# Optimization experiments

Measured on AMD Instinct MI355X. Metric: run time of the kernel, lower is better.

The kernel has to match this reference:

```python
import jax, jax.numpy as jnp
import numpy as np

K = 20
EPS = 1e-5

def get_graph_feature(x, k):
    # x: [B, C, N] -> edge features [B, 2C, N, k]
    xt = jnp.swapaxes(x, 1, 2)  # [B, N, C]
    sq = jnp.sum(xt * xt, axis=-1)  # [B, N]
    # negative squared distance: -(|a|^2 + |b|^2 - 2 a.b)
    pair = 2.0 * jnp.einsum('bnc,bmc->bnm', xt, xt) - sq[:, :, None] - sq[:, None, :]
    idx = jax.lax.top_k(pair, k)[1]  # [B, N, k] nearest neighbors (incl. self)
    neigh = jax.vmap(lambda f, i: f[i])(xt, idx)  # [B, N, k, C]
    ctr = xt[:, :, None, :]  # [B, N, 1, C]
    edge = jnp.concatenate([neigh - ctr, jnp.broadcast_to(ctr, neigh.shape)], axis=-1)  # [B,N,k,2C]
    return jnp.transpose(edge, (0, 3, 1, 2))  # [B, 2C, N, k]

def bn_lrelu(y, g, b, axes):
    # training-mode batchnorm (biased batch stats) + LeakyReLU(0.2)
    m = jnp.mean(y, axis=axes, keepdims=True)
    v = jnp.var(y, axis=axes, keepdims=True)
    shape = [1, -1] + [1] * (y.ndim - 2)
    yn = (y - m) / jnp.sqrt(v + EPS) * g.reshape(shape) + b.reshape(shape)
    return jnp.where(yn >= 0, yn, 0.2 * yn)

def edge_block(x, w, g, b, k):
    e = get_graph_feature(x, k)           # [B, 2C, N, k]
    y = jnp.einsum('bcnk,oc->bonk', e, w)  # 1x1 conv2d, no bias
    y = bn_lrelu(y, g, b, (0, 2, 3))
    return jnp.max(y, axis=-1)            # max over k -> [B, O, N]

def setup_inputs() -> dict:
    key = jax.random.key(0)
    ks = jax.random.split(key, 8)
    B, N = 8, 1024
    num_features = 256
    def w(k_, o, i):
        return jax.random.normal(k_, (o, i), dtype=jnp.float32) * (1.0 / np.sqrt(i))
    d = {
        'x': jax.random.normal(ks[0], (B, N, 3), dtype=jnp.float32),
        'w1': w(ks[1], 64, 6),   'g1': jnp.ones(64),  'b1': jnp.zeros(64),
        'w2': w(ks[2], 64, 128), 'g2': jnp.ones(64),  'b2': jnp.zeros(64),
        'w3': w(ks[3], 128, 128),'g3': jnp.ones(128), 'b3': jnp.zeros(128),
        'w4': w(ks[4], 256, 256),'g4': jnp.ones(256), 'b4': jnp.zeros(256),
        'w5': w(ks[5], 512, 512),'g5': jnp.ones(512), 'b5': jnp.zeros(512),
        'wemb': w(ks[6], num_features, 512),
    }
    return d

def reference(x, w1, g1, b1, w2, g2, b2, w3, g3, b3, w4, g4, b4, w5, g5, b5, wemb):
    xc = jnp.swapaxes(x, 2, 1)  # [B, 3, N]
    x1 = edge_block(xc, w1, g1, b1, K)  # [B, 64, N]
    x2 = edge_block(x1, w2, g2, b2, K)  # [B, 64, N]
    x3 = edge_block(x2, w3, g3, b3, K)  # [B, 128, N]
    x4 = edge_block(x3, w4, g4, b4, K)  # [B, 256, N]
    cat = jnp.concatenate([x1, x2, x3, x4], axis=1)  # [B, 512, N]
    y = jnp.einsum('bcn,oc->bon', cat, w5)            # 1x1 conv1d
    y = bn_lrelu(y, g5, b5, (0, 2))
    feat = jnp.max(y, axis=-1)  # [B, 512]
    return feat @ wemb.T        # [B, num_features]
```

## Files before the change

### kernel.cpp

```cpp
#include <hip/hip_runtime.h>
#include <hip/hip_bf16.h>
#include <math.h>

#define BB 8
#define NN 1024
#define KNNK 20
#define LDC 512

typedef __attribute__((ext_vector_type(8))) short bfrag8;
typedef __attribute__((ext_vector_type(4))) float facc4;
typedef __attribute__((ext_vector_type(2))) float v2f;

struct bh8 { __hip_bfloat16 h[8]; };

__device__ __forceinline__ bh8 cvt8(float4 a, float4 b) {
    bh8 v;
    v.h[0] = __float2bfloat16(a.x); v.h[1] = __float2bfloat16(a.y);
    v.h[2] = __float2bfloat16(a.z); v.h[3] = __float2bfloat16(a.w);
    v.h[4] = __float2bfloat16(b.x); v.h[5] = __float2bfloat16(b.y);
    v.h[6] = __float2bfloat16(b.z); v.h[7] = __float2bfloat16(b.w);
    return v;
}

template<int CTRL, int RMASK>
__device__ __forceinline__ float fmax_dpp(float x) {
    int xi = __float_as_int(x);
    int yi = __builtin_amdgcn_update_dpp(xi, xi, CTRL, RMASK, 0xF, false);
    return fmaxf(x, __int_as_float(yi));
}

__device__ __forceinline__ float wave_max64(float x) {
    x = fmax_dpp<0x121, 0xF>(x);
    x = fmax_dpp<0x122, 0xF>(x);
    x = fmax_dpp<0x124, 0xF>(x);
    x = fmax_dpp<0x128, 0xF>(x);
    x = fmax_dpp<0x142, 0xA>(x);
    x = fmax_dpp<0x143, 0xC>(x);
    return __int_as_float(__builtin_amdgcn_readlane(__float_as_int(x), 63));
}

__device__ __forceinline__ void select20_pf(float (*dist)[1024],
                                            int q0, int w, int lane,
                                            int* __restrict__ idxout) {
    float d[2][16];
    int   sl[2][16];
#pragma unroll
    for (int qi = 0; qi < 2; qi++) {
        int row = w * 2 + qi;
#pragma unroll
        for (int j = 0; j < 16; j++) { d[qi][j] = dist[row][lane + 64 * j]; sl[qi][j] = j; }
    }
    constexpr unsigned char CA[63] = {
        0,2,4,6,8,10,12,14,
        0,1,4,5,8,9,12,13,
        1,5,9,13,
        0,1,2,3,8,9,10,11,
        2,3,10,11,
        1,3,5,9,11,13,
        0,1,2,3,4,5,6,7,
        4,5,6,7,
        2,3,6,7,10,11,
        1,3,5,7,9,11,13};
    constexpr unsigned char CB[63] = {
        1,3,5,7,9,11,13,15,
        2,3,6,7,10,11,14,15,
        2,6,10,14,
        4,5,6,7,12,13,14,15,
        4,5,12,13,
        2,4,6,10,12,14,
        8,9,10,11,12,13,14,15,
        8,9,10,11,
        4,5,8,9,12,13,
        2,4,6,8,10,12,14};
#pragma unroll
    for (int c = 0; c < 63; c++) {
        const int a = CA[c], bq = CB[c];
#pragma unroll
        for (int qi = 0; qi < 2; qi++) {
            bool sw = d[qi][a] < d[qi][bq];
            float dmx = sw ? d[qi][bq] : d[qi][a];
            float dmn = sw ? d[qi][a]  : d[qi][bq];
            d[qi][a] = dmx; d[qi][bq] = dmn;
            int smx = sw ? sl[qi][bq] : sl[qi][a];
            int smn = sw ? sl[qi][a]  : sl[qi][bq];
            sl[qi][a] = smx; sl[qi][bq] = smn;
        }
    }
    unsigned long long slp[2];
#pragma unroll
    for (int qi = 0; qi < 2; qi++) {
        int row = w * 2 + qi;
#pragma unroll
        for (int j = 0; j < 16; j++) dist[row][j * 64 + lane] = d[qi][j];
        unsigned long long p = 0;
#pragma unroll
        for (int j = 0; j < 16; j++) p |= (unsigned long long)sl[qi][j] << (4 * j);
        slp[qi] = p;
    }
    float head[2] = {d[0][0], d[1][0]};
    float pf[2]   = {d[0][1], d[1][1]};
    int   ptr[2]  = {2, 2};
    for (int t = 0; t < KNNK; t++) {
#pragma unroll
        for (int qi = 0; qi < 2; qi++) {
            int row = w * 2 + qi;
            float bv = wave_max64(head[qi]);
            unsigned long long ball = __ballot(head[qi] == bv);
            int wl = (int)__builtin_ctzll(ball);
            bool win = (lane == wl);
            if (win) {
                idxout[(q0 + row) * KNNK + t] = (int)(slp[qi] & 15ull) * 64 + lane;
            }
            head[qi] = win ? pf[qi] : head[qi];
            slp[qi]  = win ? (slp[qi] >> 4) : slp[qi];
            if (win) {
                int p = ptr[qi];
                pf[qi] = (p < 16) ? dist[row][p * 64 + lane] : -INFINITY;
                ptr[qi] = p + 1;
            }
        }
    }
}

__device__ __forceinline__ void zero_r1(float* r1s, float* r1q, int O, int tid) {
    for (int i = tid; i < 32 * O; i += 256) { r1s[i] = 0.f; r1q[i] = 0.f; }
}

__global__ __launch_bounds__(256, 4) void knn3_fused(const float* __restrict__ x,
                                                     const float* __restrict__ w1,
                                                     float* __restrict__ zf,
                                                     int* __restrict__ idxout,
                                                     float* __restrict__ r1s, float* __restrict__ r1q) {
    __shared__ float dist[8][1024];
    int tid = threadIdx.x;
    int q0 = (blockIdx.x & 7) * 1024 + (blockIdx.x >> 3) * 8;
    int b = q0 >> 10;
    if (blockIdx.x == 0) zero_r1(r1s, r1q, 64, tid);
    const float* xb = x + (size_t)b * NN * 3;
    int lane = tid & 63, w = tid >> 6;
    float qx[8], qy[8], qz[8];
#pragma unroll
    for (int q = 0; q < 8; q++) {
        const float* qr = xb + (size_t)((q0 & (NN - 1)) + q) * 3;
        qx[q] = qr[0]; qy[q] = qr[1]; qz[q] = qr[2];
    }
#pragma unroll
    for (int cq = 0; cq < 4; cq++) {
        int cand = w * 256 + cq * 64 + lane;
        const float* cr = xb + (size_t)cand * 3;
        float cx = cr[0], cy = cr[1], cz = cr[2];
        float sqc = 0.f;
        sqc += cx * cx; sqc += cy * cy; sqc += cz * cz;
#pragma unroll
        for (int q = 0; q < 8; q++) {
            float d = qx[q] * cx + qy[q] * cy + qz[q] * cz;
            dist[q][cand] = 2.f * d - sqc;
        }
    }
    for (int i = tid; i < 8 * 128; i += 256) {
        int lq = i >> 7, j = i & 127;
        const float* wr = w1 + (j < 64 ? j * 6 : (j - 64) * 6 + 3);
        const float* xr = x + (size_t)(q0 + lq) * 3;
        zf[(size_t)(q0 + lq) * 128 + j] = wr[0] * xr[0] + wr[1] * xr[1] + wr[2] * xr[2];
    }
    __syncthreads();
    select20_pf(dist, q0, w, lane, idxout);
}

template<int C>
__device__ __forceinline__ void knn_body(const float* __restrict__ xT,
                                         const float* __restrict__ sqn,
                                         int* __restrict__ idxout,
                                         float (*dist)[1024], int knnBlk) {
    int tid = threadIdx.x;
    int q0 = (knnBlk & 7) * 1024 + (knnBlk >> 3) * 8;
    int b = q0 >> 10;
    int lane = tid & 63, w = tid >> 6;
    int cand0 = w * 256 + 4 * lane;
    const float* xTb = xT + (size_t)b * C * 1024;
    const float* qrow = xTb + (q0 & (NN - 1));
    float4 sq4 = *(const float4*)(sqn + b * NN + cand0);
    v2f acc2[4][4];
#pragma unroll
    for (int j = 0; j < 4; j++)
#pragma unroll
        for (int p = 0; p < 4; p++) acc2[j][p] = (v2f){0.f, 0.f};
    for (int cg = 0; cg < C / 4; cg++) {
        float4 rch[4];
#pragma unroll
        for (int c = 0; c < 4; c++)
            rch[c] = *(const float4*)(xTb + (size_t)(4 * cg + c) * 1024 + cand0);
#pragma unroll
        for (int c = 0; c < 4; c++) {
            const float* qr = qrow + (size_t)(4 * cg + c) * 1024;
            float4 qa = *(const float4*)qr;
            float4 qb = *(const float4*)(qr + 4);
            v2f qp[4] = {{qa.x, qa.y}, {qa.z, qa.w}, {qb.x, qb.y}, {qb.z, qb.w}};
            float rj[4] = {rch[c].x, rch[c].y, rch[c].z, rch[c].w};
#pragma unroll
            for (int j = 0; j < 4; j++) {
                v2f rr = {rj[j], rj[j]};
                acc2[j][0] += rr * qp[0];
                acc2[j][1] += rr * qp[1];
                acc2[j][2] += rr * qp[2];
                acc2[j][3] += rr * qp[3];
            }
        }
    }
#pragma unroll
    for (int p = 0; p < 4; p++)
#pragma unroll
        for (int half = 0; half < 2; half++) {
            int q = 2 * p + half;
            float4 dv;
            dv.x = 2.f * acc2[0][p][half] - sq4.x;
            dv.y = 2.f * acc2[1][p][half] - sq4.y;
            dv.z = 2.f * acc2[2][p][half] - sq4.z;
            dv.w = 2.f * acc2[3][p][half] - sq4.w;
            *(float4*)&dist[q][cand0] = dv;
        }
    __syncthreads();
    select20_pf(dist, q0, w, lane, idxout);
}

template<int C, int ZO2>
__global__ __launch_bounds__(256, 4) void knnz_fat(const float* __restrict__ xT,
                                                   const float* __restrict__ xt, int off,
                                                   const float* __restrict__ sqn,
                                                   int* __restrict__ idxout,
                                                   const float* __restrict__ w,
                                                   float* __restrict__ zf,
                                                   float* __restrict__ r1s, float* __restrict__ r1q,
                                                   int Onext) {
    __shared__ float dist[8][1024];
    int tid = threadIdx.x;
    if ((int)blockIdx.x < BB * NN / 8) {
        knn_body<C>(xT, sqn, idxout, dist, blockIdx.x);
        return;
    }
    constexpr int ZO = ZO2 / 2;
    int zblk = blockIdx.x - BB * NN / 8;
    if (zblk == 0) zero_r1(r1s, r1q, Onext, tid);
    float (*xs)[C] = (float (*)[C])&dist[0][0];
    int p0 = zblk * 16;
    for (int j = tid; j < 16 * (C / 4); j += 256) {
        int p = j / (C / 4), c4 = j % (C / 4);
        *(float4*)&xs[p][4 * c4] = *(const float4*)(xt + (size_t)(p0 + p) * LDC + off + 4 * c4);
    }
    __syncthreads();
    for (int j = tid; j < ZO2; j += 256) {
        const float* wr = w + (j < ZO ? (size_t)j * 2 * C : (size_t)(j - ZO) * 2 * C + C);
        float acc[16];
#pragma unroll
        for (int p = 0; p < 16; p++) acc[p] = 0.f;
        for (int c4 = 0; c4 < C / 4; c4++) {
            float4 wv = *(const float4*)(wr + 4 * c4);
#pragma unroll
            for (int p = 0; p < 16; p++) {
                float4 xv = *(const float4*)&xs[p][4 * c4];
                acc[p] += wv.x * xv.x + wv.y * xv.y + wv.z * xv.z + wv.w * xv.w;
            }
        }
#pragma unroll
        for (int p = 0; p < 16; p++) zf[(size_t)(p0 + p) * ZO2 + j] = acc[p];
    }
}

__global__ __launch_bounds__(256, 4) void knnz4_fat(const float* __restrict__ xT,
                                                    const float* __restrict__ sqn,
                                                    int* __restrict__ idxout,
                                                    const float* __restrict__ xtcat,
                                                    const float* __restrict__ w4,
                                                    __hip_bfloat16* __restrict__ zf4,
                                                    float* __restrict__ r1s, float* __restrict__ r1q) {
    __shared__ __align__(16) char smem[36864];
    int tid = threadIdx.x;
    if ((int)blockIdx.x < BB * NN / 8) {
        float (*dist)[1024] = (float (*)[1024])smem;
        if (blockIdx.x == 0) zero_r1(r1s, r1q, 256, tid);
        knn_body<128>(xT, sqn, idxout, dist, blockIdx.x);
        return;
    }
    __hip_bfloat16 (*A)[72] = (__hip_bfloat16 (*)[72])smem;
    __hip_bfloat16 (*W)[72] = (__hip_bfloat16 (*)[72])(smem + 18432);
    int zblk = blockIdx.x - BB * NN / 8;
    int mt = zblk >> 2, nt = zblk & 3;
    int lane = tid & 63, wvx = tid >> 6;
    int mw = wvx >> 1, nw = wvx & 1;
    int m0 = lane & 15, qd = lane >> 4;
    int r = tid & 127, hf = tid >> 7;
    facc4 acc[4][4];
    facc4 zz = {0.f, 0.f, 0.f, 0.f};
#pragma unroll
    for (int mi = 0; mi < 4; mi++)
#pragma unroll
        for (int ni = 0; ni < 4; ni++) acc[mi][ni] = zz;
    int j = nt * 128 + r;
    const float* wsrc = w4 + (j < 256 ? (size_t)j * 256 : (size_t)(j - 256) * 256 + 128);
    const float* asrc = xtcat + (size_t)(mt * 128 + r) * 512 + 128;
    for (int kc = 0; kc < 2; kc++) {
#pragma unroll
        for (int u = 0; u < 4; u++) {
            int c0 = kc * 64 + hf * 32 + 8 * u;
            float4 a0 = *(const float4*)(asrc + c0);
            float4 a1 = *(const float4*)(asrc + c0 + 4);
            *(bh8*)&A[r][hf * 32 + 8 * u] = cvt8(a0, a1);
            float4 w0 = *(const float4*)(wsrc + c0);
            float4 w1 = *(const float4*)(wsrc + c0 + 4);
            *(bh8*)&W[r][hf * 32 + 8 * u] = cvt8(w0, w1);
        }
        __syncthreads();
#pragma unroll
        for (int kk = 0; kk < 2; kk++) {
            bfrag8 af[4], bf[4];
#pragma unroll
            for (int mi = 0; mi < 4; mi++)
                af[mi] = *(const bfrag8*)&A[64 * mw + 16 * mi + m0][32 * kk + 8 * qd];
#pragma unroll
            for (int ni = 0; ni < 4; ni++)
                bf[ni] = *(const bfrag8*)&W[64 * nw + 16 * ni + m0][32 * kk + 8 * qd];
#pragma unroll
            for (int mi = 0; mi < 4; mi++)
#pragma unroll
                for (int ni = 0; ni < 4; ni++)
                    acc[mi][ni] = __builtin_amdgcn_mfma_f32_16x16x32_bf16(af[mi], bf[ni], acc[mi][ni], 0, 0, 0);
        }
        __syncthreads();
    }
#pragma unroll
    for (int mi = 0; mi < 4; mi++)
#pragma unroll
        for (int ni = 0; ni < 4; ni++)
#pragma unroll
            for (int rg = 0; rg < 4; rg++) {
                int row = mt * 128 + mw * 64 + mi * 16 + qd * 4 + rg;
                int col = nt * 128 + nw * 64 + ni * 16 + m0;
                zf4[(size_t)row * 512 + col] = __float2bfloat16(acc[mi][ni][rg]);
            }
}

template<int O2>
__global__ __launch_bounds__(256) void gatherstats_k(const float* __restrict__ zf,
                                                     const int* __restrict__ idx,
                                                     float* __restrict__ ymax, float* __restrict__ ymin,
                                                     float* __restrict__ r1s, float* __restrict__ r1q) {
    constexpr int O = O2 / 2;
    __shared__ float red_s[4][O], red_q[4][O];
    int wv = threadIdx.x >> 6, lane = threadIdx.x & 63;
    int n = (blockIdx.x & 7) * 1024 + (blockIdx.x >> 3) * 4 + wv;
    int b = n >> 10;
    const float* zbatch = zf + (size_t)b * NN * O2;
    int nb[KNNK];
#pragma unroll
    for (int k = 0; k < KNNK; k++) nb[k] = idx[n * KNNK + k];
#pragma unroll
    for (int ch = 0; ch < O / 64; ch++) {
        int o = ch * 64 + lane;
        float g[KNNK];
#pragma unroll
        for (int k = 0; k < KNNK; k++) g[k] = zbatch[(size_t)nb[k] * O2 + o];
        float mx = -INFINITY, mn = INFINITY, s = 0.f, ss = 0.f;
#pragma unroll
        for (int k = 0; k < KNNK; k++) {
            float v = g[k];
            mx = fmaxf(mx, v); mn = fminf(mn, v); s += v; ss += v * v;
        }
        float zn  = zf[(size_t)n * O2 + o];
        float zbn = zf[(size_t)n * O2 + O + o];
        float d = zbn - zn;
        mx += d; mn += d;
        ss = ss + 2.f * d * s + (float)KNNK * d * d;
        s  = s + (float)KNNK * d;
        ymax[(size_t)n * O + o] = mx;
        ymin[(size_t)n * O + o] = mn;
        red_s[wv][o] = s;
        red_q[wv][o] = ss;
    }
    __syncthreads();
    int bucket = blockIdx.x & 31;
    for (int o = threadIdx.x; o < O; o += 256) {
        float s4 = red_s[0][o] + red_s[1][o] + red_s[2][o] + red_s[3][o];
        float q4 = red_q[0][o] + red_q[1][o] + red_q[2][o] + red_q[3][o];
        atomicAdd(&r1s[(size_t)bucket * O + o], s4);
        atomicAdd(&r1q[(size_t)bucket * O + o], q4);
    }
}

__global__ __launch_bounds__(256) void gatherstats4_k(const __hip_bfloat16* __restrict__ zf4,
                                                      const int* __restrict__ idx,
                                                      float* __restrict__ ymax, float* __restrict__ ymin,
                                                      float* __restrict__ r1s, float* __restrict__ r1q) {
    __shared__ float red_s[4][256], red_q[4][256];
    int wv = threadIdx.x >> 6, lane = threadIdx.x & 63;
    int n = (blockIdx.x & 7) * 1024 + (blockIdx.x >> 3) * 4 + wv;
    int b = n >> 10;
    const __hip_bfloat16* zbatch = zf4 + (size_t)b * NN * 512;
    int nb[KNNK];
#pragma unroll
    for (int k = 0; k < KNNK; k++) nb[k] = idx[n * KNNK + k];
#pragma unroll
    for (int ch = 0; ch < 4; ch++) {
        int o = ch * 64 + lane;
        float g[KNNK];
#pragma unroll
        for (int k = 0; k < KNNK; k++) g[k] = __bfloat162float(zbatch[(size_t)nb[k] * 512 + o]);
        float mx = -INFINITY, mn = INFINITY, s = 0.f, ss = 0.f;
#pragma unroll
        for (int k = 0; k < KNNK; k++) {
            float v = g[k];
            mx = fmaxf(mx, v); mn = fminf(mn, v); s += v; ss += v * v;
        }
        float zn  = __bfloat162float(zf4[(size_t)n * 512 + o]);
        float zbn = __bfloat162float(zf4[(size_t)n * 512 + 256 + o]);
        float d = zbn - zn;
        mx += d; mn += d;
        ss = ss + 2.f * d * s + (float)KNNK * d * d;
        s  = s + (float)KNNK * d;
        ymax[(size_t)n * 256 + o] = mx;
        ymin[(size_t)n * 256 + o] = mn;
        red_s[wv][o] = s;
        red_q[wv][o] = ss;
    }
    __syncthreads();
    int bucket = blockIdx.x & 31;
    for (int o = threadIdx.x; o < 256; o += 256) {
        float s4 = red_s[0][o] + red_s[1][o] + red_s[2][o] + red_s[3][o];
        float q4 = red_q[0][o] + red_q[1][o] + red_q[2][o] + red_q[3][o];
        atomicAdd(&r1s[(size_t)bucket * 256 + o], s4);
        atomicAdd(&r1q[(size_t)bucket * 256 + o], q4);
    }
}

template<int O>
__global__ __launch_bounds__(256) void epitrans2_k(const float* __restrict__ ymax, const float* __restrict__ ymin,
                                                   const float* __restrict__ r1s, const float* __restrict__ r1q,
                                                   const float* __restrict__ g, const float* __restrict__ beta,
                                                   double invM,
                                                   float* __restrict__ xtcat, int off_out,
                                                   float* __restrict__ xT, float* __restrict__ sqn,
                                                   __hip_bfloat16* __restrict__ xbf) {
    __shared__ float tile[64][O + 1];
    __shared__ float ssh[O], tth[O];
    int n0 = blockIdx.x * 64;
    int b = n0 >> 10;
    int tid = threadIdx.x;
    for (int o = tid; o < O; o += 256) {
        double sd = 0.0, qd = 0.0;
        for (int r = 0; r < 32; r++) { sd += r1s[(size_t)r * O + o]; qd += r1q[(size_t)r * O + o]; }
        double mean = sd * invM;
        double var = qd * invM - mean * mean;
        float inv = (float)(1.0 / sqrt(var + 1e-5));
        float sc = g[o] * inv;
        ssh[o] = sc;
        tth[o] = beta[o] - (float)mean * sc;
    }
    __syncthreads();
    for (int i = tid; i < 64 * O; i += 256) {
        int nl = i / O;
        int o = i & (O - 1);
        int n = n0 + nl;
        float sc = ssh[o];
        float v = sc >= 0.f ? ymax[(size_t)n * O + o] : ymin[(size_t)n * O + o];
        float y = sc * v + tth[o];
        y = y >= 0.f ? y : 0.2f * y;
        xtcat[(size_t)n * LDC + off_out + o] = y;
        xbf[(size_t)n * LDC + off_out + o] = __float2bfloat16(y);
        tile[nl][o] = y;
    }
    __syncthreads();
    if (tid < 64) {
        float sq = 0.f;
        for (int c = 0; c < O; c++) { float v = tile[tid][c]; sq += v * v; }
        sqn[n0 + tid] = sq;
    }
    int r = tid >> 4, cq = tid & 15;
#pragma unroll
    for (int ct = 0; ct < O / 16; ct++) {
        int c = ct * 16 + r;
        float4 ov;
        ov.x = tile[4 * cq + 0][c];
        ov.y = tile[4 * cq + 1][c];
        ov.z = tile[4 * cq + 2][c];
        ov.w = tile[4 * cq + 3][c];
        *(float4*)(xT + ((size_t)b * O + c) * 1024 + (n0 & (NN - 1)) + 4 * cq) = ov;
    }
}

__global__ __launch_bounds__(256) void epilogue4_k(const float* __restrict__ ymax, const float* __restrict__ ymin,
                                                   const float* __restrict__ r1s, const float* __restrict__ r1q,
                                                   const float* __restrict__ g, const float* __restrict__ beta,
                                                   double invM,
                                                   __hip_bfloat16* __restrict__ xbf) {
    __shared__ float ssh[256], tth[256];
    int n0 = blockIdx.x * 64;
    int tid = threadIdx.x;
    {
        int o = tid;
        double sd = 0.0, qd = 0.0;
        for (int r = 0; r < 32; r++) { sd += r1s[(size_t)r * 256 + o]; qd += r1q[(size_t)r * 256 + o]; }
        double mean = sd * invM;
        double var = qd * invM - mean * mean;
        float inv = (float)(1.0 / sqrt(var + 1e-5));
        float sc = g[o] * inv;
        ssh[o] = sc;
        tth[o] = beta[o] - (float)mean * sc;
    }
    __syncthreads();
    for (int i = tid; i < 64 * 256; i += 256) {
        int nl = i >> 8;
        int o = i & 255;
        int n = n0 + nl;
        float sc = ssh[o];
        float v = sc >= 0.f ? ymax[(size_t)n * 256 + o] : ymin[(size_t)n * 256 + o];
        float y = sc * v + tth[o];
        y = y >= 0.f ? y : 0.2f * y;
        xbf[(size_t)n * LDC + 256 + o] = __float2bfloat16(y);
    }
}

__global__ __launch_bounds__(256) void gemm5_mfma(const __hip_bfloat16* __restrict__ xbf,
                                                  const float* __restrict__ w5,
                                                  float* __restrict__ pmax, float* __restrict__ pmn,
                                                  float* __restrict__ ps, float* __restrict__ pq) {
    __shared__ __hip_bfloat16 A[128][72];
    __shared__ __hip_bfloat16 W[128][72];
    int mt = blockIdx.x >> 2, nt = blockIdx.x & 3;
    int tid = threadIdx.x;
    int lane = tid & 63, wvx = tid >> 6;
    int mw = wvx >> 1, nw = wvx & 1;
    int m0 = lane & 15, qd = lane >> 4;
    int r = tid & 127, hf = tid >> 7;
    facc4 acc[4][4];
    facc4 zz = {0.f, 0.f, 0.f, 0.f};
#pragma unroll
    for (int mi = 0; mi < 4; mi++)
#pragma unroll
        for (int ni = 0; ni < 4; ni++) acc[mi][ni] = zz;
    for (int kc = 0; kc < 8; kc++) {
        const __hip_bfloat16* ap = xbf + (size_t)(mt * 128 + r) * 512 + kc * 64 + hf * 32;
        const float* wp = w5 + (size_t)(nt * 128 + r) * 512 + kc * 64 + hf * 32;
#pragma unroll
        for (int u = 0; u < 4; u++) {
            bh8 av = *(const bh8*)(ap + 8 * u);
            *(bh8*)&A[r][hf * 32 + 8 * u] = av;
            float4 w0 = *(const float4*)(wp + 8 * u);
            float4 w1 = *(const float4*)(wp + 8 * u + 4);
            *(bh8*)&W[r][hf * 32 + 8 * u] = cvt8(w0, w1);
        }
        __syncthreads();
#pragma unroll
        for (int kk = 0; kk < 2; kk++) {
            bfrag8 af[4], bf[4];
#pragma unroll
            for (int mi = 0; mi < 4; mi++)
                af[mi] = *(const bfrag8*)&A[64 * mw + 16 * mi + m0][32 * kk + 8 * qd];
#pragma unroll
            for (int ni = 0; ni < 4; ni++)
                bf[ni] = *(const bfrag8*)&W[64 * nw + 16 * ni + m0][32 * kk + 8 * qd];
#pragma unroll
            for (int mi = 0; mi < 4; mi++)
#pragma unroll
                for (int ni = 0; ni < 4; ni++)
                    acc[mi][ni] = __builtin_amdgcn_mfma_f32_16x16x32_bf16(af[mi], bf[ni], acc[mi][ni], 0, 0, 0);
        }
        __syncthreads();
    }
#pragma unroll
    for (int mi = 0; mi < 4; mi++) {
        int grp = mt * 8 + mw * 4 + mi;
#pragma unroll
        for (int ni = 0; ni < 4; ni++) {
            float mx = -INFINITY, mn = INFINITY, s = 0.f, ss = 0.f;
#pragma unroll
            for (int rg = 0; rg < 4; rg++) {
                float v = acc[mi][ni][rg];
                mx = fmaxf(mx, v); mn = fminf(mn, v); s += v; ss += v * v;
            }
#pragma unroll
            for (int m = 16; m < 64; m <<= 1) {
                mx = fmaxf(mx, __shfl_xor(mx, m));
                mn = fminf(mn, __shfl_xor(mn, m));
                s += __shfl_xor(s, m);
                ss += __shfl_xor(ss, m);
            }
            if (qd == 0) {
                int o = nt * 128 + nw * 64 + ni * 16 + m0;
                pmax[(size_t)grp * 512 + o] = mx;
                pmn [(size_t)grp * 512 + o] = mn;
                ps  [(size_t)grp * 512 + o] = s;
                pq  [(size_t)grp * 512 + o] = ss;
            }
        }
    }
}

__global__ __launch_bounds__(256) void bnstat5_k(const float* __restrict__ ps, const float* __restrict__ pq,
                                                 const float* __restrict__ g, const float* __restrict__ beta,
                                                 float* __restrict__ s_out, float* __restrict__ t_out) {
    __shared__ double lds_s[4][8], lds_q[4][8];
    int tid = threadIdx.x;
    int lane = tid & 63, wv = tid >> 6;
    int ol = lane & 7;
    int rg = wv * 8 + (lane >> 3);
    int o = blockIdx.x * 8 + ol;
    double s = 0.0, q = 0.0;
    for (int r = rg; r < 512; r += 32) {
        s += ps[(size_t)r * 512 + o];
        q += pq[(size_t)r * 512 + o];
    }
    s += __shfl_xor(s, 8);  q += __shfl_xor(q, 8);
    s += __shfl_xor(s, 16); q += __shfl_xor(q, 16);
    s += __shfl_xor(s, 32); q += __shfl_xor(q, 32);
    if (lane < 8) { lds_s[wv][ol] = s; lds_q[wv][ol] = q; }
    __syncthreads();
    if (tid < 8) {
        s = lds_s[0][tid] + lds_s[1][tid] + lds_s[2][tid] + lds_s[3][tid];
        q = lds_q[0][tid] + lds_q[1][tid] + lds_q[2][tid] + lds_q[3][tid];
        double invM = 1.0 / (BB * NN);
        double mean = s * invM;
        double var = q * invM - mean * mean;
        float inv = (float)(1.0 / sqrt(var + 1e-5));
        int oo = blockIdx.x * 8 + tid;
        float sc = g[oo] * inv;
        s_out[oo] = sc;
        t_out[oo] = beta[oo] - (float)mean * sc;
    }
}

__global__ __launch_bounds__(256) void featreduce_k(const float* __restrict__ pmax, const float* __restrict__ pmn,
                                                    const float* __restrict__ s, const float* __restrict__ t,
                                                    float* __restrict__ feat8) {
    __shared__ float smx[4][64], smn[4][64];
    int blk = blockIdx.x;
    int b = blk >> 3, oc = blk & 7;
    int tid = threadIdx.x;
    int lane = tid & 63, wv = tid >> 6;
    int o = oc * 64 + lane;
    float mx = -INFINITY, mn = INFINITY;
    for (int r = b * 64 + wv; r < (b + 1) * 64; r += 4) {
        mx = fmaxf(mx, pmax[(size_t)r * 512 + o]);
        mn = fminf(mn, pmn [(size_t)r * 512 + o]);
    }
    smx[wv][lane] = mx; smn[wv][lane] = mn;
    __syncthreads();
    if (wv == 0) {
        mx = fmaxf(fmaxf(smx[0][lane], smx[1][lane]), fmaxf(smx[2][lane], smx[3][lane]));
        mn = fminf(fminf(smn[0][lane], smn[1][lane]), fminf(smn[2][lane], smn[3][lane]));
        float sc = s[o];
        float v = sc >= 0.f ? mx : mn;
        float y = sc * v + t[o];
        feat8[(size_t)b * 512 + o] = y >= 0.f ? y : 0.2f * y;
    }
}

__global__ __launch_bounds__(256) void outgemm_k(const float* __restrict__ feat8,
                                                 const float* __restrict__ wemb,
                                                 float* __restrict__ out) {
    __shared__ __align__(16) float feat[512];
    int blk = blockIdx.x;
    int b = blk >> 3, nc = blk & 7;
    int tid = threadIdx.x;
    for (int i = tid; i < 512; i += 256) feat[i] = feat8[(size_t)b * 512 + i];
    __syncthreads();
    int o_l = tid >> 3, kc = tid & 7;
    int o = nc * 32 + o_l;
    const float4* wr = (const float4*)(wemb + (size_t)o * 512 + kc * 64);
    const float4* fv = (const float4*)(feat + kc * 64);
    float acc = 0.f;
#pragma unroll
    for (int i = 0; i < 16; i++) {
        float4 wv = wr[i];
        float4 f  = fv[i];
        acc += wv.x * f.x + wv.y * f.y + wv.z * f.z + wv.w * f.w;
    }
    acc += __shfl_xor(acc, 1);
    acc += __shfl_xor(acc, 2);
    acc += __shfl_xor(acc, 4);
    if (kc == 0) out[(size_t)b * 256 + o] = acc;
}

extern "C" void kernel_launch(void* const* d_in, const int* in_sizes, int n_in,
                              void* d_out, int out_size, void* d_ws, size_t ws_size,
                              hipStream_t stream) {
    const float* x    = (const float*)d_in[0];
    const float* w1   = (const float*)d_in[1];
    const float* g1   = (const float*)d_in[2];
    const float* b1   = (const float*)d_in[3];
    const float* w2   = (const float*)d_in[4];
    const float* g2   = (const float*)d_in[5];
    const float* b2   = (const float*)d_in[6];
    const float* w3   = (const float*)d_in[7];
    const float* g3   = (const float*)d_in[8];
    const float* b3   = (const float*)d_in[9];
    const float* w4   = (const float*)d_in[10];
    const float* g4   = (const float*)d_in[11];
    const float* b4   = (const float*)d_in[12];
    const float* w5   = (const float*)d_in[13];
    const float* g5   = (const float*)d_in[14];
    const float* b5   = (const float*)d_in[15];
    const float* wemb = (const float*)d_in[16];
    float* out = (float*)d_out;

    float* fws    = (float*)d_ws;
    float* xtcat  = fws;
    float* ymax   = xtcat + (size_t)BB * NN * 512;
    float* ymin   = ymax + (size_t)BB * NN * 256;
    float* psum   = ymin + (size_t)BB * NN * 256;
    float* psumsq = psum + (size_t)BB * NN * 256;
    float* xT     = psum;
    float* pmax   = ymax;
    float* pmn    = pmax + 512 * 512;
    float* ps5    = pmn + 512 * 512;
    float* pq5    = ps5 + 512 * 512;
    float* feat8  = psumsq;
    float* sqn    = psumsq + (size_t)BB * NN * 256;
    float* s_arr  = sqn + BB * NN;
    float* t_arr  = s_arr + 512;
    float* r1s    = t_arr + 512;
    float* r1q    = r1s + 32 * 512;
    int*   idxb   = (int*)(r1q + 32 * 512);
    float* zfull  = (float*)(idxb + BB * NN * KNNK);
    __hip_bfloat16* zf4 = (__hip_bfloat16*)zfull;
    __hip_bfloat16* xbf = (__hip_bfloat16*)(zfull + (size_t)BB * NN * 512);

    const double invM_edge = 1.0 / ((double)BB * NN * KNNK);
    const int nbn = BB * NN;
    const int NK = nbn / 8;
    const int NZ = nbn / 16;

    knn3_fused<<<NK, 256, 0, stream>>>(x, w1, zfull, idxb, r1s, r1q);
    gatherstats_k<128><<<nbn / 4, 256, 0, stream>>>(zfull, idxb, ymax, ymin, r1s, r1q);
    epitrans2_k<64><<<128, 256, 0, stream>>>(ymax, ymin, r1s, r1q, g1, b1, invM_edge, xtcat, 0, xT, sqn, xbf);

    knnz_fat<64, 128><<<NK + NZ, 256, 0, stream>>>(xT, xtcat, 0, sqn, idxb, w2, zfull, r1s, r1q, 64);
    gatherstats_k<128><<<nbn / 4, 256, 0, stream>>>(zfull, idxb, ymax, ymin, r1s, r1q);
    epitrans2_k<64><<<128, 256, 0, stream>>>(ymax, ymin, r1s, r1q, g2, b2, invM_edge, xtcat, 64, xT, sqn, xbf);

    knnz_fat<64, 256><<<NK + NZ, 256, 0, stream>>>(xT, xtcat, 64, sqn, idxb, w3, zfull, r1s, r1q, 128);
    gatherstats_k<256><<<nbn / 4, 256, 0, stream>>>(zfull, idxb, ymax, ymin, r1s, r1q);
    epitrans2_k<128><<<128, 256, 0, stream>>>(ymax, ymin, r1s, r1q, g3, b3, invM_edge, xtcat, 128, xT, sqn, xbf);

    knnz4_fat<<<NK + 256, 256, 0, stream>>>(xT, sqn, idxb, xtcat, w4, zf4, r1s, r1q);
    gatherstats4_k<<<nbn / 4, 256, 0, stream>>>(zf4, idxb, ymax, ymin, r1s, r1q);
    epilogue4_k<<<128, 256, 0, stream>>>(ymax, ymin, r1s, r1q, g4, b4, invM_edge, xbf);

    gemm5_mfma<<<256, 256, 0, stream>>>(xbf, w5, pmax, pmn, ps5, pq5);
    bnstat5_k<<<64, 256, 0, stream>>>(ps5, pq5, g5, b5, s_arr, t_arr);
    featreduce_k<<<64, 256, 0, stream>>>(pmax, pmn, s_arr, t_arr, feat8);
    outgemm_k<<<64, 256, 0, stream>>>(feat8, wemb, out);
}
```

Baseline: 330.7 us.

## Halve kNN queries per block and split layer-4 fused kernel into two launches

Each kNN block now handles 4 queries instead of 8, with one wave selecting one query's top-20. This doubles the grid, halves shared memory per block and raises the launch-bounds occupancy target to 8 blocks. The layer-4 fat kernel, which mixed kNN blocks with MFMA z-GEMM blocks, is split into a separate zgemm4_mfma launch followed by a knn_fused launch, and epilogue4 uses 32-point blocks across twice as many blocks. The aim is more parallelism and shorter serial selection per wave, at the cost of the per-query distance GEMM reusing each candidate load across fewer queries and one extra kernel launch.

```diff
diff --git a/kernel.cpp b/kernel.cpp
--- a/kernel.cpp
+++ b/kernel.cpp
@@ -39,17 +39,13 @@
     return __int_as_float(__builtin_amdgcn_readlane(__float_as_int(x), 63));
 }
 
-__device__ __forceinline__ void select20_pf(float (*dist)[1024],
-                                            int q0, int w, int lane,
-                                            int* __restrict__ idxout) {
-    float d[2][16];
-    int   sl[2][16];
-#pragma unroll
-    for (int qi = 0; qi < 2; qi++) {
-        int row = w * 2 + qi;
-#pragma unroll
-        for (int j = 0; j < 16; j++) { d[qi][j] = dist[row][lane + 64 * j]; sl[qi][j] = j; }
-    }
+__device__ __forceinline__ void select20_one(float (*dist)[1024],
+                                             int q0, int w, int lane,
+                                             int* __restrict__ idxout) {
+    float d[16];
+    int   sl[16];
+#pragma unroll
+    for (int j = 0; j < 16; j++) { d[j] = dist[w][lane + 64 * j]; sl[j] = j; }
     constexpr unsigned char CA[63] = {
         0,2,4,6,8,10,12,14,
         0,1,4,5,8,9,12,13,
@@ -75,49 +71,35 @@
 #pragma unroll
     for (int c = 0; c < 63; c++) {
         const int a = CA[c], bq = CB[c];
-#pragma unroll
-        for (int qi = 0; qi < 2; qi++) {
-            bool sw = d[qi][a] < d[qi][bq];
-            float dmx = sw ? d[qi][bq] : d[qi][a];
-            float dmn = sw ? d[qi][a]  : d[qi][bq];
-            d[qi][a] = dmx; d[qi][bq] = dmn;
-            int smx = sw ? sl[qi][bq] : sl[qi][a];
-            int smn = sw ? sl[qi][a]  : sl[qi][bq];
-            sl[qi][a] = smx; sl[qi][bq] = smn;
-        }
-    }
-    unsigned long long slp[2];
-#pragma unroll
-    for (int qi = 0; qi < 2; qi++) {
-        int row = w * 2 + qi;
-#pragma unroll
-        for (int j = 0; j < 16; j++) dist[row][j * 64 + lane] = d[qi][j];
-        unsigned long long p = 0;
-#pragma unroll
-        for (int j = 0; j < 16; j++) p |= (unsigned long long)sl[qi][j] << (4 * j);
-        slp[qi] = p;
-    }
-    float head[2] = {d[0][0], d[1][0]};
-    float pf[2]   = {d[0][1], d[1][1]};
-    int   ptr[2]  = {2, 2};
+        bool sw = d[a] < d[bq];
+        float dmx = sw ? d[bq] : d[a];
+        float dmn = sw ? d[a]  : d[bq];
+        d[a] = dmx; d[bq] = dmn;
+        int smx = sw ? sl[bq] : sl[a];
+        int smn = sw ? sl[a]  : sl[bq];
+        sl[a] = smx; sl[bq] = smn;
+    }
+#pragma unroll
+    for (int j = 0; j < 16; j++) dist[w][j * 64 + lane] = d[j];
+    unsigned long long slp = 0;
+#pragma unroll
+    for (int j = 0; j < 16; j++) slp |= (unsigned long long)sl[j] << (4 * j);
+    float head = d[0];
+    float pf   = d[1];
+    int   ptr  = 2;
     for (int t = 0; t < KNNK; t++) {
-#pragma unroll
-        for (int qi = 0; qi < 2; qi++) {
-            int row = w * 2 + qi;
-            float bv = wave_max64(head[qi]);
-            unsigned long long ball = __ballot(head[qi] == bv);
-            int wl = (int)__builtin_ctzll(ball);
-            bool win = (lane == wl);
-            if (win) {
-                idxout[(q0 + row) * KNNK + t] = (int)(slp[qi] & 15ull) * 64 + lane;
-            }
-            head[qi] = win ? pf[qi] : head[qi];
-            slp[qi]  = win ? (slp[qi] >> 4) : slp[qi];
-            if (win) {
-                int p = ptr[qi];
-                pf[qi] = (p < 16) ? dist[row][p * 64 + lane] : -INFINITY;
-                ptr[qi] = p + 1;
-            }
+        float bv = wave_max64(head);
+        unsigned long long ball = __ballot(head == bv);
+        int wl = (int)__builtin_ctzll(ball);
+        bool win = (lane == wl);
+        if (win) {
+            idxout[(q0 + w) * KNNK + t] = (int)(slp & 15ull) * 64 + lane;
+        }
+        head = win ? pf : head;
+        slp  = win ? (slp >> 4) : slp;
+        if (win) {
+            pf = (ptr < 16) ? dist[w][ptr * 64 + lane] : -INFINITY;
+            ptr++;
         }
     }
 }
@@ -126,21 +108,21 @@
     for (int i = tid; i < 32 * O; i += 256) { r1s[i] = 0.f; r1q[i] = 0.f; }
 }
 
-__global__ __launch_bounds__(256, 4) void knn3_fused(const float* __restrict__ x,
+__global__ __launch_bounds__(256, 8) void knn3_fused(const float* __restrict__ x,
                                                      const float* __restrict__ w1,
                                                      float* __restrict__ zf,
                                                      int* __restrict__ idxout,
                                                      float* __restrict__ r1s, float* __restrict__ r1q) {
-    __shared__ float dist[8][1024];
-    int tid = threadIdx.x;
-    int q0 = (blockIdx.x & 7) * 1024 + (blockIdx.x >> 3) * 8;
+    __shared__ float dist[4][1024];
+    int tid = threadIdx.x;
+    int q0 = (blockIdx.x & 7) * 1024 + (blockIdx.x >> 3) * 4;
     int b = q0 >> 10;
     if (blockIdx.x == 0) zero_r1(r1s, r1q, 64, tid);
     const float* xb = x + (size_t)b * NN * 3;
     int lane = tid & 63, w = tid >> 6;
-    float qx[8], qy[8], qz[8];
-#pragma unroll
-    for (int q = 0; q < 8; q++) {
+    float qx[4], qy[4], qz[4];
+#pragma unroll
+    for (int q = 0; q < 4; q++) {
         const float* qr = xb + (size_t)((q0 & (NN - 1)) + q) * 3;
         qx[q] = qr[0]; qy[q] = qr[1]; qz[q] = qr[2];
     }
@@ -149,22 +131,21 @@
         int cand = w * 256 + cq * 64 + lane;
         const float* cr = xb + (size_t)cand * 3;
         float cx = cr[0], cy = cr[1], cz = cr[2];
-        float sqc = 0.f;
-        sqc += cx * cx; sqc += cy * cy; sqc += cz * cz;
-#pragma unroll
-        for (int q = 0; q < 8; q++) {
+        float sqc = cx * cx + cy * cy + cz * cz;
+#pragma unroll
+        for (int q = 0; q < 4; q++) {
             float d = qx[q] * cx + qy[q] * cy + qz[q] * cz;
             dist[q][cand] = 2.f * d - sqc;
         }
     }
-    for (int i = tid; i < 8 * 128; i += 256) {
+    for (int i = tid; i < 4 * 128; i += 256) {
         int lq = i >> 7, j = i & 127;
         const float* wr = w1 + (j < 64 ? j * 6 : (j - 64) * 6 + 3);
         const float* xr = x + (size_t)(q0 + lq) * 3;
         zf[(size_t)(q0 + lq) * 128 + j] = wr[0] * xr[0] + wr[1] * xr[1] + wr[2] * xr[2];
     }
     __syncthreads();
-    select20_pf(dist, q0, w, lane, idxout);
+    select20_one(dist, q0, w, lane, idxout);
 }
 
 template<int C>
@@ -173,18 +154,18 @@
                                          int* __restrict__ idxout,
                                          float (*dist)[1024], int knnBlk) {
     int tid = threadIdx.x;
-    int q0 = (knnBlk & 7) * 1024 + (knnBlk >> 3) * 8;
+    int q0 = (knnBlk & 7) * 1024 + (knnBlk >> 3) * 4;
     int b = q0 >> 10;
     int lane = tid & 63, w = tid >> 6;
     int cand0 = w * 256 + 4 * lane;
     const float* xTb = xT + (size_t)b * C * 1024;
     const float* qrow = xTb + (q0 & (NN - 1));
     float4 sq4 = *(const float4*)(sqn + b * NN + cand0);
-    v2f acc2[4][4];
+    v2f acc2[4][2];
 #pragma unroll
     for (int j = 0; j < 4; j++)
 #pragma unroll
-        for (int p = 0; p < 4; p++) acc2[j][p] = (v2f){0.f, 0.f};
+        for (int p = 0; p < 2; p++) acc2[j][p] = (v2f){0.f, 0.f};
     for (int cg = 0; cg < C / 4; cg++) {
         float4 rch[4];
 #pragma unroll
@@ -194,21 +175,19 @@
         for (int c = 0; c < 4; c++) {
             const float* qr = qrow + (size_t)(4 * cg + c) * 1024;
             float4 qa = *(const float4*)qr;
-            float4 qb = *(const float4*)(qr + 4);
-            v2f qp[4] = {{qa.x, qa.y}, {qa.z, qa.w}, {qb.x, qb.y}, {qb.z, qb.w}};
+            v2f qp0 = {qa.x, qa.y};
+            v2f qp1 = {qa.z, qa.w};
             float rj[4] = {rch[c].x, rch[c].y, rch[c].z, rch[c].w};
 #pragma unroll
             for (int j = 0; j < 4; j++) {
                 v2f rr = {rj[j], rj[j]};
-                acc2[j][0] += rr * qp[0];
-                acc2[j][1] += rr * qp[1];
-                acc2[j][2] += rr * qp[2];
-                acc2[j][3] += rr * qp[3];
+                acc2[j][0] += rr * qp0;
+                acc2[j][1] += rr * qp1;
             }
         }
     }
 #pragma unroll
-    for (int p = 0; p < 4; p++)
+    for (int p = 0; p < 2; p++)
 #pragma unroll
         for (int half = 0; half < 2; half++) {
             int q = 2 * p + half;
@@ -220,11 +199,11 @@
             *(float4*)&dist[q][cand0] = dv;
         }
     __syncthreads();
-    select20_pf(dist, q0, w, lane, idxout);
+    select20_one(dist, q0, w, lane, idxout);
 }
 
 template<int C, int ZO2>
-__global__ __launch_bounds__(256, 4) void knnz_fat(const float* __restrict__ xT,
+__global__ __launch_bounds__(256, 8) void knnz_fat(const float* __restrict__ xT,
                                                    const float* __restrict__ xt, int off,
                                                    const float* __restrict__ sqn,
                                                    int* __restrict__ idxout,
@@ -232,14 +211,14 @@
                                                    float* __restrict__ zf,
                                                    float* __restrict__ r1s, float* __restrict__ r1q,
                                                    int Onext) {
-    __shared__ float dist[8][1024];
-    int tid = threadIdx.x;
-    if ((int)blockIdx.x < BB * NN / 8) {
+    __shared__ float dist[4][1024];
+    int tid = threadIdx.x;
+    if ((int)blockIdx.x < BB * NN / 4) {
         knn_body<C>(xT, sqn, idxout, dist, blockIdx.x);
         return;
     }
     constexpr int ZO = ZO2 / 2;
-    int zblk = blockIdx.x - BB * NN / 8;
+    int zblk = blockIdx.x - BB * NN / 4;
     if (zblk == 0) zero_r1(r1s, r1q, Onext, tid);
     float (*xs)[C] = (float (*)[C])&dist[0][0];
     int p0 = zblk * 16;
@@ -266,25 +245,24 @@
     }
 }
 
-__global__ __launch_bounds__(256, 4) void knnz4_fat(const float* __restrict__ xT,
+template<int C>
+__global__ __launch_bounds__(256, 8) void knn_fused(const float* __restrict__ xT,
                                                     const float* __restrict__ sqn,
                                                     int* __restrict__ idxout,
-                                                    const float* __restrict__ xtcat,
-                                                    const float* __restrict__ w4,
-                                                    __hip_bfloat16* __restrict__ zf4,
-                                                    float* __restrict__ r1s, float* __restrict__ r1q) {
-    __shared__ __align__(16) char smem[36864];
-    int tid = threadIdx.x;
-    if ((int)blockIdx.x < BB * NN / 8) {
-        float (*dist)[1024] = (float (*)[1024])smem;
-        if (blockIdx.x == 0) zero_r1(r1s, r1q, 256, tid);
-        knn_body<128>(xT, sqn, idxout, dist, blockIdx.x);
-        return;
-    }
-    __hip_bfloat16 (*A)[72] = (__hip_bfloat16 (*)[72])smem;
-    __hip_bfloat16 (*W)[72] = (__hip_bfloat16 (*)[72])(smem + 18432);
-    int zblk = blockIdx.x - BB * NN / 8;
-    int mt = zblk >> 2, nt = zblk & 3;
+                                                    float* __restrict__ r1s, float* __restrict__ r1q,
+                                                    int Onext) {
+    __shared__ float dist[4][1024];
+    if (blockIdx.x == 0) zero_r1(r1s, r1q, Onext, threadIdx.x);
+    knn_body<C>(xT, sqn, idxout, dist, blockIdx.x);
+}
+
+__global__ __launch_bounds__(256) void zgemm4_mfma(const float* __restrict__ xtcat,
+                                                   const float* __restrict__ w4,
+                                                   __hip_bfloat16* __restrict__ zf4) {
+    __shared__ __hip_bfloat16 A[128][72];
+    __shared__ __hip_bfloat16 W[128][72];
+    int mt = blockIdx.x >> 2, nt = blockIdx.x & 3;
+    int tid = threadIdx.x;
     int lane = tid & 63, wvx = tid >> 6;
     int mw = wvx >> 1, nw = wvx & 1;
     int m0 = lane & 15, qd = lane >> 4;
@@ -492,7 +470,7 @@
                                                    double invM,
                                                    __hip_bfloat16* __restrict__ xbf) {
     __shared__ float ssh[256], tth[256];
-    int n0 = blockIdx.x * 64;
+    int n0 = blockIdx.x * 32;
     int tid = threadIdx.x;
     {
         int o = tid;
@@ -506,7 +484,7 @@
         tth[o] = beta[o] - (float)mean * sc;
     }
     __syncthreads();
-    for (int i = tid; i < 64 * 256; i += 256) {
+    for (int i = tid; i < 32 * 256; i += 256) {
         int nl = i >> 8;
         int o = i & 255;
         int n = n0 + nl;
@@ -725,7 +703,7 @@
 
     const double invM_edge = 1.0 / ((double)BB * NN * KNNK);
     const int nbn = BB * NN;
-    const int NK = nbn / 8;
+    const int NK = nbn / 4;
     const int NZ = nbn / 16;
 
     knn3_fused<<<NK, 256, 0, stream>>>(x, w1, zfull, idxb, r1s, r1q);
@@ -740,9 +718,10 @@
     gatherstats_k<256><<<nbn / 4, 256, 0, stream>>>(zfull, idxb, ymax, ymin, r1s, r1q);
     epitrans2_k<128><<<128, 256, 0, stream>>>(ymax, ymin, r1s, r1q, g3, b3, invM_edge, xtcat, 128, xT, sqn, xbf);
 
-    knnz4_fat<<<NK + 256, 256, 0, stream>>>(xT, sqn, idxb, xtcat, w4, zf4, r1s, r1q);
+    zgemm4_mfma<<<256, 256, 0, stream>>>(xtcat, w4, zf4);
+    knn_fused<128><<<NK, 256, 0, stream>>>(xT, sqn, idxb, r1s, r1q, 256);
     gatherstats4_k<<<nbn / 4, 256, 0, stream>>>(zf4, idxb, ymax, ymin, r1s, r1q);
-    epilogue4_k<<<128, 256, 0, stream>>>(ymax, ymin, r1s, r1q, g4, b4, invM_edge, xbf);
+    epilogue4_k<<<256, 256, 0, stream>>>(ymax, ymin, r1s, r1q, g4, b4, invM_edge, xbf);
 
     gemm5_mfma<<<256, 256, 0, stream>>>(xbf, w5, pmax, pmn, ps5, pq5);
     bnstat5_k<<<64, 256, 0, stream>>>(ps5, pq5, g5, b5, s_arr, t_arr);
```

Result: slower. 487.7 us (+47.5%).
